# Kernel tuning notes

Hardware: AMD Instinct MI355X
Metric: run time of the kernel (lower is better)

Reference implementation:

```python
import math
import jax, jax.numpy as jnp
import numpy as np
from jax import lax

# ---- fixed (non-learned) kernels, built exactly as in Canny.__init__ ----
def _sobel_2d(k=5):
    r = np.linspace(-(k // 2), k // 2, k).astype(np.float32)
    x, y = np.meshgrid(r, r, indexing='ij')
    den = x ** 2 + y ** 2
    den[:, k // 2] = 1.0
    return (x / den / 6.0).astype(np.float32)

_S = _sobel_2d(5)
W_SY = jnp.asarray(_S.reshape(1, 1, 5, 5))            # sobel_y weight
W_SX = jnp.asarray(_S.T.reshape(1, 1, 5, 5))          # sobel_x weight (transposed)

_pos = [(0, 1), (2, 1), (1, 0), (1, 2), (0, 0), (2, 2), (0, 2), (2, 0)]
_ksel = np.zeros((8, 1, 3, 3), dtype=np.float32)
for _i, (_a, _b) in enumerate(_pos):
    _ksel[_i, 0, _a, _b] = 1.0
W_SEL = jnp.asarray(_ksel)
SEL_IDS = jnp.asarray(np.array([[0, 1], [4, 5], [2, 3], [6, 7],
                                [0, 1], [4, 5], [2, 3], [6, 7]], dtype=np.int32))
W_HYST = jnp.ones((1, 1, 3, 3), dtype=jnp.float32)

_DN = ('NCHW', 'OIHW', 'NCHW')

def _conv_reflect(x, w, pad):
    x = jnp.pad(x, ((0, 0), (0, 0), (pad, pad), (pad, pad)), mode='reflect')
    return lax.conv_general_dilated(x, w, (1, 1), 'VALID', dimension_numbers=_DN)

def _conv_zero(x, w, pad):
    return lax.conv_general_dilated(x, w, (1, 1), ((pad, pad), (pad, pad)),
                                    dimension_numbers=_DN)

THRESH_LO = 0.1
THRESH_HI = 0.1

def setup_inputs() -> dict:
    key = jax.random.key(0)
    images = jax.random.uniform(key, (16, 3, 512, 512), dtype=jnp.float32)
    return {'images': images}

def reference(images):
    # shift from [-1,1] to [0,1] if needed
    images = jnp.where(images.min() < -0.001, (images + 1.0) * 0.5, images)
    # channel L2 norm -> [B,1,H,W], normalize by global max
    mag = jnp.linalg.norm(images, axis=1, keepdims=True)
    mag = mag / mag.max()
    sobel_x = _conv_reflect(mag, W_SX, 2)
    sobel_y = _conv_reflect(mag, W_SY, 2)
    grad_mag = jnp.sqrt(sobel_x ** 2 + sobel_y ** 2)             # [B,1,H,W]
    phase = jnp.arctan2(sobel_x, sobel_y + 1e-5)
    phase = jnp.mod(jnp.round(phase / (math.pi / 4)) + 4.0, 8.0).astype(jnp.int32)
    selections = _conv_zero(grad_mag, W_SEL, 1)                  # [B,8,H,W]
    neb_ids = SEL_IDS[phase[:, 0]]                               # [B,H,W,2]
    nebs = jnp.take_along_axis(selections, jnp.transpose(neb_ids, (0, 3, 1, 2)), axis=1)
    # phase-dependent non-maximum suppression
    mask = (grad_mag <= nebs[:, 0:1]) | (grad_mag < nebs[:, 1:2])
    grad_mag = jnp.where(mask, 0.0, grad_mag)
    # low threshold
    grad_mag = jnp.where(grad_mag < THRESH_LO, 0.0, grad_mag)
    # hysteresis
    weak_mask = (grad_mag < THRESH_HI) & (grad_mag > THRESH_LO)
    high_mask = grad_mag > THRESH_HI
    high_nebs = _conv_reflect(high_mask.astype(jnp.float32), W_HYST, 1)
    weak_keep = weak_mask & (high_nebs > 0)
    kill = (~weak_keep) & (~high_mask)
    grad_mag = jnp.where(kill, 0.0, grad_mag)
    # String_Finder: binarize edges at 0.1
    b_edges = jnp.where(grad_mag > 0.1, 1.0, 0.0)
    sobel = jnp.concatenate([sobel_y, sobel_x], axis=1)          # [B,2,H,W]
    return b_edges, sobel
```

## Files before the change

### kernel.cpp

```cpp
#include <hip/hip_runtime.h>
#include <math.h>

#define HH 512
#define WW 512
#define HW (HH*WW)

__device__ __forceinline__ int refl(int i) {
  if (i < 0) return -i;
  if (i >= HH) return 2*HH - 2 - i;
  return i;
}

__device__ __forceinline__ float sumsq3(float r, float g, float b) {
  return __fadd_rn(__fadd_rn(__fmul_rn(r,r), __fmul_rn(g,g)), __fmul_rn(b,b));
}

__global__ __launch_bounds__(256) void k1_sumsq(const float* __restrict__ img,
                                                float* __restrict__ ss,
                                                float* __restrict__ partials) {
  int gid = blockIdx.x * 256 + threadIdx.x;
  int n  = gid >> 16;
  int p4 = gid & 65535;
  const float* base = img + (size_t)n * 3 * HW;
  float4 r = ((const float4*)(base        ))[p4];
  float4 g = ((const float4*)(base +   HW ))[p4];
  float4 b = ((const float4*)(base + 2*HW ))[p4];
  float4 s;
  s.x = sumsq3(r.x, g.x, b.x);
  s.y = sumsq3(r.y, g.y, b.y);
  s.z = sumsq3(r.z, g.z, b.z);
  s.w = sumsq3(r.w, g.w, b.w);
  ((float4*)ss)[gid] = s;

  float m = fmaxf(fmaxf(s.x, s.y), fmaxf(s.z, s.w));
  #pragma unroll
  for (int off = 32; off > 0; off >>= 1)
    m = fmaxf(m, __shfl_down(m, off));
  __shared__ float sm[4];
  int lane = threadIdx.x & 63, wv = threadIdx.x >> 6;
  if (lane == 0) sm[wv] = m;
  __syncthreads();
  if (threadIdx.x == 0)
    partials[blockIdx.x] = fmaxf(fmaxf(sm[0], sm[1]), fmaxf(sm[2], sm[3]));
}

__global__ __launch_bounds__(256) void k1b_reduce(const float* __restrict__ partials,
                                                  float* __restrict__ ssmax) {
  float m = 0.0f;
  #pragma unroll
  for (int i = 0; i < 16; ++i)
    m = fmaxf(m, partials[threadIdx.x + 256 * i]);
  #pragma unroll
  for (int off = 32; off > 0; off >>= 1)
    m = fmaxf(m, __shfl_down(m, off));
  __shared__ float sm[4];
  int lane = threadIdx.x & 63, wv = threadIdx.x >> 6;
  if (lane == 0) sm[wv] = m;
  __syncthreads();
  if (threadIdx.x == 0)
    ssmax[0] = fmaxf(fmaxf(sm[0], sm[1]), fmaxf(sm[2], sm[3]));
}

__global__ __launch_bounds__(256) void k3_sobel(const float* __restrict__ ss,
                                                const float* __restrict__ ssmax,
                                                float* __restrict__ sobel_out,
                                                float* __restrict__ gm,
                                                unsigned char* __restrict__ pairb) {
  __shared__ float magS[20 * 68];
  int tx = threadIdx.x;
  int ty = threadIdx.y;
  int x0 = blockIdx.x * 64;
  int y0 = blockIdx.y * 16;
  int n  = blockIdx.z;
  const float* sp = ss + (size_t)n * HW;
  float mm = sqrtf(ssmax[0]);

  int tid = ty * 64 + tx;
  for (int i = tid; i < 20 * 68; i += 256) {
    int r = i / 68, c = i - r * 68;
    int gy = refl(y0 - 2 + r);
    int gx = refl(x0 - 2 + c);
    magS[i] = __fdiv_rn(sqrtf(sp[gy * WW + gx]), mm);
  }
  __syncthreads();

  const double wA0 = (double)(-2.0f/8.0f/6.0f);
  const double wA1 = (double)(-2.0f/5.0f/6.0f);
  const double wA2 = (double)(-2.0f/1.0f/6.0f);
  const double wB0 = (double)(-1.0f/5.0f/6.0f);
  const double wB1 = (double)(-1.0f/2.0f/6.0f);
  const double wB2 = (double)(-1.0f/1.0f/6.0f);

  double S[8], T[8], C[8], D0[8], D1[8];
  #pragma unroll
  for (int j = 0; j < 8; ++j) {
    const float* rowp = &magS[(4 * ty + j) * 68 + tx];
    double v0 = (double)rowp[0], v1 = (double)rowp[1], v2 = (double)rowp[2],
           v3 = (double)rowp[3], v4 = (double)rowp[4];
    S[j]  = v0 + v4;  T[j]  = v1 + v3;  C[j] = v2;
    D0[j] = v0 - v4;  D1[j] = v1 - v3;
  }

  int x = x0 + tx;
  #pragma unroll
  for (int dy = 0; dy < 4; ++dy) {
    int r = 4 * ty + dy;
    int y = y0 + r;
    int j = dy;
    double asy = wA0*(S[j]-S[j+4]) + wA1*(T[j]-T[j+4]) + wA2*(C[j]-C[j+4])
               + wB0*(S[j+1]-S[j+3]) + wB1*(T[j+1]-T[j+3]) + wB2*(C[j+1]-C[j+3]);
    double asx = wA0*(D0[j]+D0[j+4]) + wA1*(D0[j+1]+D0[j+3]) + wA2*D0[j+2]
               + wB0*(D1[j]+D1[j+4]) + wB1*(D1[j+1]+D1[j+3]) + wB2*D1[j+2];
    float fsy = (float)asy, fsx = (float)asx;
    int p = y * WW + x;
    sobel_out[(size_t)n * 2 * HW + p]      = fsy;
    sobel_out[(size_t)n * 2 * HW + HW + p] = fsx;
    float g = sqrtf(__fadd_rn(__fmul_rn(fsx, fsx), __fmul_rn(fsy, fsy)));
    gm[(size_t)n * HW + p] = g;
    float ph = atan2f(fsx, __fadd_rn(fsy, 1e-5f));
    float pf = __fdiv_rn(ph, 0.78539816339744830962f);
    float rr = rintf(pf);
    int ip = ((int)rr + 4) & 7;
    pairb[(size_t)n * HW + p] = (unsigned char)(ip & 3);
  }
}

__global__ __launch_bounds__(256) void k4_nms(const float* __restrict__ gm,
                                              const unsigned char* __restrict__ pairb,
                                              float* __restrict__ edges) {
  int x = blockIdx.x * 64 + threadIdx.x;
  int y = blockIdx.y * 4  + threadIdx.y;
  int n = blockIdx.z;
  const float* gp = gm + (size_t)n * HW;
  int p = y * WW + x;
  float g = gp[p];
  int pr = pairb[(size_t)n * HW + p];
  const int dy0[4] = {-1, -1,  0, -1};
  const int dx0[4] = { 0, -1, -1,  1};
  const int dy1[4] = { 1,  1,  0,  1};
  const int dx1[4] = { 0,  1,  1, -1};
  int y0 = y + dy0[pr], x0 = x + dx0[pr];
  int y1 = y + dy1[pr], x1 = x + dx1[pr];
  float n0 = (y0 >= 0 && y0 < HH && x0 >= 0 && x0 < WW) ? gp[y0 * WW + x0] : 0.0f;
  float n1 = (y1 >= 0 && y1 < HH && x1 >= 0 && x1 < WW) ? gp[y1 * WW + x1] : 0.0f;
  bool mask = (g <= n0) || (g < n1);
  edges[(size_t)n * HW + p] = (!mask && (g > 0.1f)) ? 1.0f : 0.0f;
}

extern "C" void kernel_launch(void* const* d_in, const int* in_sizes, int n_in,
                              void* d_out, int out_size, void* d_ws, size_t ws_size,
                              hipStream_t stream) {
  const float* img = (const float*)d_in[0];
  float* out = (float*)d_out;
  char* ws = (char*)d_ws;

  float* ssmax    = (float*)ws;
  float* partials = (float*)(ws + 256);
  float* ssbuf    = (float*)(ws + 256 + 16384);
  float* gm       = (float*)(ws + 256 + 16384 + 16777216);
  unsigned char* pairb = (unsigned char*)(ws + 256 + 16384 + 2*16777216);

  float* edges = out;
  float* sobel = out + 4194304;

  k1_sumsq  <<<dim3(4096), dim3(256), 0, stream>>>(img, ssbuf, partials);
  k1b_reduce<<<dim3(1),    dim3(256), 0, stream>>>(partials, ssmax);
  k3_sobel<<<dim3(8, 32, 16), dim3(64, 4), 0, stream>>>(ssbuf, ssmax, sobel, gm, pairb);
  k4_nms  <<<dim3(8, 128, 16), dim3(64, 4), 0, stream>>>(gm, pairb, edges);
}
```

Measured before the change: 131.1 us.

## Fuse sumsq, sobel and NMS into one tiled kernel and drop intermediates

The max-reduction kernel no longer writes the sum-of-squares buffer; the sobel kernel recomputes magnitudes directly from the image with a wider halo, computes gradient magnitude into shared memory over an extended tile, and performs non-maximum suppression in-block, eliminating the gm and phase-pair global buffers and the separate NMS kernel. This removes substantial intermediate global traffic and one launch, at the cost of re-reading the image with scalar loads, halo recomputation, and losing per-thread vertical register reuse in the double-precision stencil.

```diff
diff --git a/kernel.cpp b/kernel.cpp
--- a/kernel.cpp
+++ b/kernel.cpp
@@ -15,24 +15,25 @@
   return __fadd_rn(__fadd_rn(__fmul_rn(r,r), __fmul_rn(g,g)), __fmul_rn(b,b));
 }
 
-__global__ __launch_bounds__(256) void k1_sumsq(const float* __restrict__ img,
-                                                float* __restrict__ ss,
-                                                float* __restrict__ partials) {
-  int gid = blockIdx.x * 256 + threadIdx.x;
-  int n  = gid >> 16;
-  int p4 = gid & 65535;
-  const float* base = img + (size_t)n * 3 * HW;
-  float4 r = ((const float4*)(base        ))[p4];
-  float4 g = ((const float4*)(base +   HW ))[p4];
-  float4 b = ((const float4*)(base + 2*HW ))[p4];
-  float4 s;
-  s.x = sumsq3(r.x, g.x, b.x);
-  s.y = sumsq3(r.y, g.y, b.y);
-  s.z = sumsq3(r.z, g.z, b.z);
-  s.w = sumsq3(r.w, g.w, b.w);
-  ((float4*)ss)[gid] = s;
-
-  float m = fmaxf(fmaxf(s.x, s.y), fmaxf(s.z, s.w));
+__global__ __launch_bounds__(256) void k1_max(const float* __restrict__ img,
+                                              float* __restrict__ partials) {
+  int t = blockIdx.x * 256 + threadIdx.x;
+  float m = 0.0f;
+  #pragma unroll
+  for (int i = 0; i < 2; ++i) {
+    int gid = t + i * 524288;
+    int n  = gid >> 16;
+    int p4 = gid & 65535;
+    const float* base = img + (size_t)n * 3 * HW;
+    float4 r = ((const float4*)(base        ))[p4];
+    float4 g = ((const float4*)(base +   HW ))[p4];
+    float4 b = ((const float4*)(base + 2*HW ))[p4];
+    float sx = sumsq3(r.x, g.x, b.x);
+    float sy = sumsq3(r.y, g.y, b.y);
+    float sz = sumsq3(r.z, g.z, b.z);
+    float sw = sumsq3(r.w, g.w, b.w);
+    m = fmaxf(m, fmaxf(fmaxf(sx, sy), fmaxf(sz, sw)));
+  }
   #pragma unroll
   for (int off = 32; off > 0; off >>= 1)
     m = fmaxf(m, __shfl_down(m, off));
@@ -48,7 +49,7 @@
                                                   float* __restrict__ ssmax) {
   float m = 0.0f;
   #pragma unroll
-  for (int i = 0; i < 16; ++i)
+  for (int i = 0; i < 8; ++i)
     m = fmaxf(m, partials[threadIdx.x + 256 * i]);
   #pragma unroll
   for (int off = 32; off > 0; off >>= 1)
@@ -61,26 +62,28 @@
     ssmax[0] = fmaxf(fmaxf(sm[0], sm[1]), fmaxf(sm[2], sm[3]));
 }
 
-__global__ __launch_bounds__(256) void k3_sobel(const float* __restrict__ ss,
+__global__ __launch_bounds__(256) void k3_fused(const float* __restrict__ img,
                                                 const float* __restrict__ ssmax,
                                                 float* __restrict__ sobel_out,
-                                                float* __restrict__ gm,
-                                                unsigned char* __restrict__ pairb) {
-  __shared__ float magS[20 * 68];
-  int tx = threadIdx.x;
-  int ty = threadIdx.y;
+                                                float* __restrict__ edges) {
+  __shared__ float magS[22 * 72];
+  __shared__ float gmS[18 * 68];
+  __shared__ unsigned char pairS[16 * 64];
+
+  int tid = threadIdx.y * 64 + threadIdx.x;
   int x0 = blockIdx.x * 64;
   int y0 = blockIdx.y * 16;
   int n  = blockIdx.z;
-  const float* sp = ss + (size_t)n * HW;
+  const float* base = img + (size_t)n * 3 * HW;
   float mm = sqrtf(ssmax[0]);
 
-  int tid = ty * 64 + tx;
-  for (int i = tid; i < 20 * 68; i += 256) {
-    int r = i / 68, c = i - r * 68;
-    int gy = refl(y0 - 2 + r);
-    int gx = refl(x0 - 2 + c);
-    magS[i] = __fdiv_rn(sqrtf(sp[gy * WW + gx]), mm);
+  for (int i = tid; i < 22 * 70; i += 256) {
+    int r = i / 70, c = i - r * 70;
+    int gy = refl(y0 - 3 + r);
+    int gx = refl(x0 - 3 + c);
+    int gp = gy * WW + gx;
+    float ssv = sumsq3(base[gp], base[HW + gp], base[2 * HW + gp]);
+    magS[r * 72 + c] = __fdiv_rn(sqrtf(ssv), mm);
   }
   __syncthreads();
 
@@ -91,60 +94,56 @@
   const double wB1 = (double)(-1.0f/2.0f/6.0f);
   const double wB2 = (double)(-1.0f/1.0f/6.0f);
 
-  double S[8], T[8], C[8], D0[8], D1[8];
-  #pragma unroll
-  for (int j = 0; j < 8; ++j) {
-    const float* rowp = &magS[(4 * ty + j) * 68 + tx];
-    double v0 = (double)rowp[0], v1 = (double)rowp[1], v2 = (double)rowp[2],
-           v3 = (double)rowp[3], v4 = (double)rowp[4];
-    S[j]  = v0 + v4;  T[j]  = v1 + v3;  C[j] = v2;
-    D0[j] = v0 - v4;  D1[j] = v1 - v3;
+  for (int i = tid; i < 18 * 66; i += 256) {
+    int gr = i / 66, gc = i - gr * 66;
+    double S[5], T[5], C[5], D0[5], D1[5];
+    #pragma unroll
+    for (int a = 0; a < 5; ++a) {
+      const float* rowp = &magS[(gr + a) * 72 + gc];
+      double v0 = (double)rowp[0], v1 = (double)rowp[1], v2 = (double)rowp[2],
+             v3 = (double)rowp[3], v4 = (double)rowp[4];
+      S[a]  = v0 + v4;  T[a]  = v1 + v3;  C[a] = v2;
+      D0[a] = v0 - v4;  D1[a] = v1 - v3;
+    }
+    double asy = wA0*(S[0]-S[4]) + wA1*(T[0]-T[4]) + wA2*(C[0]-C[4])
+               + wB0*(S[1]-S[3]) + wB1*(T[1]-T[3]) + wB2*(C[1]-C[3]);
+    double asx = wA0*(D0[0]+D0[4]) + wA1*(D0[1]+D0[3]) + wA2*D0[2]
+               + wB0*(D1[0]+D1[4]) + wB1*(D1[1]+D1[3]) + wB2*D1[2];
+    float fsy = (float)asy, fsx = (float)asx;
+    float g = sqrtf(__fadd_rn(__fmul_rn(fsx, fsx), __fmul_rn(fsy, fsy)));
+    gmS[gr * 68 + gc] = g;
+    int cy = gr - 1, cx = gc - 1;
+    if (cy >= 0 && cy < 16 && cx >= 0 && cx < 64) {
+      size_t p = (size_t)n * 2 * HW + (size_t)(y0 + cy) * WW + (x0 + cx);
+      sobel_out[p]      = fsy;
+      sobel_out[p + HW] = fsx;
+      float ph = atan2f(fsx, __fadd_rn(fsy, 1e-5f));
+      float pf = __fdiv_rn(ph, 0.78539816339744830962f);
+      float rr = rintf(pf);
+      int ip = ((int)rr + 4) & 7;
+      pairS[cy * 64 + cx] = (unsigned char)(ip & 3);
+    }
   }
+  __syncthreads();
 
-  int x = x0 + tx;
-  #pragma unroll
-  for (int dy = 0; dy < 4; ++dy) {
-    int r = 4 * ty + dy;
-    int y = y0 + r;
-    int j = dy;
-    double asy = wA0*(S[j]-S[j+4]) + wA1*(T[j]-T[j+4]) + wA2*(C[j]-C[j+4])
-               + wB0*(S[j+1]-S[j+3]) + wB1*(T[j+1]-T[j+3]) + wB2*(C[j+1]-C[j+3]);
-    double asx = wA0*(D0[j]+D0[j+4]) + wA1*(D0[j+1]+D0[j+3]) + wA2*D0[j+2]
-               + wB0*(D1[j]+D1[j+4]) + wB1*(D1[j+1]+D1[j+3]) + wB2*D1[j+2];
-    float fsy = (float)asy, fsx = (float)asx;
-    int p = y * WW + x;
-    sobel_out[(size_t)n * 2 * HW + p]      = fsy;
-    sobel_out[(size_t)n * 2 * HW + HW + p] = fsx;
-    float g = sqrtf(__fadd_rn(__fmul_rn(fsx, fsx), __fmul_rn(fsy, fsy)));
-    gm[(size_t)n * HW + p] = g;
-    float ph = atan2f(fsx, __fadd_rn(fsy, 1e-5f));
-    float pf = __fdiv_rn(ph, 0.78539816339744830962f);
-    float rr = rintf(pf);
-    int ip = ((int)rr + 4) & 7;
-    pairb[(size_t)n * HW + p] = (unsigned char)(ip & 3);
-  }
-}
-
-__global__ __launch_bounds__(256) void k4_nms(const float* __restrict__ gm,
-                                              const unsigned char* __restrict__ pairb,
-                                              float* __restrict__ edges) {
-  int x = blockIdx.x * 64 + threadIdx.x;
-  int y = blockIdx.y * 4  + threadIdx.y;
-  int n = blockIdx.z;
-  const float* gp = gm + (size_t)n * HW;
-  int p = y * WW + x;
-  float g = gp[p];
-  int pr = pairb[(size_t)n * HW + p];
   const int dy0[4] = {-1, -1,  0, -1};
   const int dx0[4] = { 0, -1, -1,  1};
   const int dy1[4] = { 1,  1,  0,  1};
   const int dx1[4] = { 0,  1,  1, -1};
-  int y0 = y + dy0[pr], x0 = x + dx0[pr];
-  int y1 = y + dy1[pr], x1 = x + dx1[pr];
-  float n0 = (y0 >= 0 && y0 < HH && x0 >= 0 && x0 < WW) ? gp[y0 * WW + x0] : 0.0f;
-  float n1 = (y1 >= 0 && y1 < HH && x1 >= 0 && x1 < WW) ? gp[y1 * WW + x1] : 0.0f;
-  bool mask = (g <= n0) || (g < n1);
-  edges[(size_t)n * HW + p] = (!mask && (g > 0.1f)) ? 1.0f : 0.0f;
+  for (int i = tid; i < 16 * 64; i += 256) {
+    int cy = i >> 6, cx = i & 63;
+    int y = y0 + cy, x = x0 + cx;
+    float g = gmS[(cy + 1) * 68 + (cx + 1)];
+    int pr = pairS[cy * 64 + cx];
+    int yA = y + dy0[pr], xA = x + dx0[pr];
+    int yB = y + dy1[pr], xB = x + dx1[pr];
+    float n0 = (yA >= 0 && yA < HH && xA >= 0 && xA < WW)
+             ? gmS[(cy + 1 + dy0[pr]) * 68 + (cx + 1 + dx0[pr])] : 0.0f;
+    float n1 = (yB >= 0 && yB < HH && xB >= 0 && xB < WW)
+             ? gmS[(cy + 1 + dy1[pr]) * 68 + (cx + 1 + dx1[pr])] : 0.0f;
+    bool mask = (g <= n0) || (g < n1);
+    edges[(size_t)n * HW + (size_t)y * WW + x] = (!mask && (g > 0.1f)) ? 1.0f : 0.0f;
+  }
 }
 
 extern "C" void kernel_launch(void* const* d_in, const int* in_sizes, int n_in,
@@ -156,15 +155,11 @@
 
   float* ssmax    = (float*)ws;
   float* partials = (float*)(ws + 256);
-  float* ssbuf    = (float*)(ws + 256 + 16384);
-  float* gm       = (float*)(ws + 256 + 16384 + 16777216);
-  unsigned char* pairb = (unsigned char*)(ws + 256 + 16384 + 2*16777216);
 
   float* edges = out;
   float* sobel = out + 4194304;
 
-  k1_sumsq  <<<dim3(4096), dim3(256), 0, stream>>>(img, ssbuf, partials);
+  k1_max    <<<dim3(2048), dim3(256), 0, stream>>>(img, partials);
   k1b_reduce<<<dim3(1),    dim3(256), 0, stream>>>(partials, ssmax);
-  k3_sobel<<<dim3(8, 32, 16), dim3(64, 4), 0, stream>>>(ssbuf, ssmax, sobel, gm, pairb);
-  k4_nms  <<<dim3(8, 128, 16), dim3(64, 4), 0, stream>>>(gm, pairb, edges);
+  k3_fused  <<<dim3(8, 32, 16), dim3(64, 4), 0, stream>>>(img, ssmax, sobel, edges);
 }
```

Result: no change. 133.7 us (+1.9%).
